# Performance work log

Hardware: AMD Instinct MI355X
Metric: run time of the kernel (lower is better)

The kernel has to match this reference:

```python
import jax, jax.numpy as jnp
import numpy as np

DECAY = 0.99
EPS = 1e-5


def setup_inputs() -> dict:
    key = jax.random.key(0)
    k1, k2 = jax.random.split(key)
    inp = jax.random.normal(k1, (32, 64, 64, 64), dtype=jnp.float32)  # [B,H,W,dim]
    embed = jax.random.normal(k2, (64, 512), dtype=jnp.float32)       # [dim, n_embed]
    cluster_size = jnp.zeros((512,), dtype=jnp.float32)
    embed_avg = embed  # buffer initialized as embed.clone() in torch
    return {"input": inp, "embed": embed, "cluster_size": cluster_size, "embed_avg": embed_avg}


def reference(input, embed, cluster_size, embed_avg):
    dim, n_embed = embed.shape
    flatten = input.reshape(-1, dim)  # [N, dim]

    # pairwise squared distances via ||f||^2 - 2 f.E + ||E||^2 -> [N, n_embed]
    dist = ((flatten ** 2).sum(1, keepdims=True)
            - 2.0 * flatten @ embed
            + (embed ** 2).sum(0, keepdims=True))
    embed_ind_flat = jnp.argmin(dist, axis=1)  # [N] (== argmax of -dist)

    # codebook lookup (F.embedding on embed.T)
    quantize = jnp.take(embed.T, embed_ind_flat, axis=0).reshape(input.shape)

    # EMA stats: one-hot sum and one-hot @ flatten expressed as scatter-adds
    ones = jnp.ones_like(embed_ind_flat, dtype=flatten.dtype)
    embed_onehot_sum = jax.ops.segment_sum(ones, embed_ind_flat, num_segments=n_embed)      # [n_embed]
    embed_sum = jax.ops.segment_sum(flatten, embed_ind_flat, num_segments=n_embed).T       # [dim, n_embed]

    new_cluster_size = cluster_size * DECAY + (1.0 - DECAY) * embed_onehot_sum
    new_embed_avg = embed_avg * DECAY + (1.0 - DECAY) * embed_sum
    n = new_cluster_size.sum()
    cs = (new_cluster_size + EPS) / (n + n_embed * EPS) * n
    new_embed = new_embed_avg / cs[None, :]

    diff = ((jax.lax.stop_gradient(quantize) - input) ** 2).mean()
    quantize_st = input + jax.lax.stop_gradient(quantize - input)  # straight-through
    embed_ind = embed_ind_flat.reshape(input.shape[:-1])

    return (quantize_st, diff, embed_ind, new_cluster_size, new_embed_avg, new_embed)
```

## Files before the change

kernel.cpp:

```cpp
#include <hip/hip_runtime.h>

typedef __attribute__((ext_vector_type(8))) short short8_t;
typedef __attribute__((ext_vector_type(4))) float f32x4;

#define N_ROWS   131072
#define DIM      64
#define NE       512
#define DECAYF   0.99f
#define OMDECAY  0.01f
#define EPSF     1e-5f
#define GAP_THR  0.02f

#define Q_OFF    0
#define DIFF_OFF 8388608
#define IND_OFF  8388609
#define CS_OFF   8519681
#define AVG_OFF  8520193
#define EMB_OFF  8552961

#define WS_ET      0
#define WS_ENORM   32768
#define WS_EN64    33280
#define WS_CSDIV   34304
#define WS_DIFF    34816
#define WS_RCNT    34817
#define WS_IDX     34818
#define WS_RLIST   165890
#define WS_BH      296964
#define WS_BL      313348
#define WS_HIST    329732
#define WS_BINBASE 330244
#define WS_CURSOR  330756
#define WS_SORTED  331268
#define WS_ACCUM   462340

__device__ __forceinline__ ushort f32_to_bf16_rn(float f) {
    unsigned u = __float_as_uint(f);
    unsigned r = (u + 0x7FFFu + ((u >> 16) & 1u)) >> 16;
    return (ushort)r;
}
__device__ __forceinline__ float bf16_to_f32(ushort h) {
    return __uint_as_float(((unsigned)h) << 16);
}

__global__ __launch_bounds__(512) void prep1_kernel(const float* __restrict__ embed,
                                                    float* __restrict__ ws) {
    const int d = blockIdx.x;
    const int c = threadIdx.x;
    float v = embed[d * NE + c];
    ws[WS_ET + c * DIM + d] = v;

    ushort hb = f32_to_bf16_rn(v);
    float  lf = v - bf16_to_f32(hb);
    ushort lb = f32_to_bf16_rn(lf);

    const int T  = c >> 4;
    const int n  = c & 15;
    const int s  = d >> 5;
    const int k8 = (d >> 3) & 3;
    const int j  = d & 7;
    const int l  = k8 * 16 + n;
    const int idx = (T * 2 + s) * 512 + l * 8 + j;
    ((ushort*)(ws + WS_BH))[idx] = hb;
    ((ushort*)(ws + WS_BL))[idx] = lb;

    if (d == 0 && c == 0) {
        ws[WS_DIFF] = 0.0f;
        ((int*)ws)[WS_RCNT] = 0;
    }
    if (d == 1) ((int*)ws)[WS_HIST + c] = 0;
    ws[WS_ACCUM + blockIdx.x * 512 + threadIdx.x] = 0.0f;
}

__global__ __launch_bounds__(256) void prep2_kernel(float* __restrict__ ws) {
    const int jcode = blockIdx.x * 4 + (threadIdx.x >> 6);
    const int d     = threadIdx.x & 63;
    float v = ws[WS_ET + jcode * DIM + d];
    double sq = (double)v * (double)v;
    #pragma unroll
    for (int off = 32; off > 0; off >>= 1) sq += __shfl_down(sq, off, 64);
    if (d == 0) {
        ws[WS_ENORM + jcode] = (float)sq;
        ((double*)(ws + WS_EN64))[jcode] = sq;
    }
}

__global__ __launch_bounds__(256) void dist_kernel(const float* __restrict__ input,
                                                   float* __restrict__ ws) {
    const int tid  = threadIdx.x;
    const int lane = tid & 63;
    const int wv   = tid >> 6;
    const int r0   = blockIdx.x * 128 + wv * 32;
    const int n15  = lane & 15;
    const int koff = (lane >> 4) * 8;

    short8_t Ahi[2][2], Alo[2][2];
    #pragma unroll
    for (int sub = 0; sub < 2; sub++) {
        const float* rp = input + (size_t)(r0 + sub * 16 + n15) * DIM + koff;
        #pragma unroll
        for (int s = 0; s < 2; s++) {
            float4 x0 = *(const float4*)(rp + s * 32);
            float4 x1 = *(const float4*)(rp + s * 32 + 4);
            float xf[8] = {x0.x, x0.y, x0.z, x0.w, x1.x, x1.y, x1.z, x1.w};
            short8_t h, l;
            #pragma unroll
            for (int e = 0; e < 8; e++) {
                ushort hb = f32_to_bf16_rn(xf[e]);
                float  lf = xf[e] - bf16_to_f32(hb);
                ushort lb = f32_to_bf16_rn(lf);
                h[e] = (short)hb;
                l[e] = (short)lb;
            }
            Ahi[sub][s] = h;
            Alo[sub][s] = l;
        }
    }

    const ushort* bhp = (const ushort*)(ws + WS_BH) + lane * 8;
    const ushort* blp = (const ushort*)(ws + WS_BL) + lane * 8;

    float m1[8], m2[8];
    int   j1[8];
    #pragma unroll
    for (int i = 0; i < 8; i++) { m1[i] = 3.4e38f; m2[i] = 3.4e38f; j1[i] = 0; }

    #pragma unroll 2
    for (int T = 0; T < 32; T++) {
        short8_t Bh0 = *(const short8_t*)(bhp + T * 1024);
        short8_t Bh1 = *(const short8_t*)(bhp + T * 1024 + 512);
        short8_t Bl0 = *(const short8_t*)(blp + T * 1024);
        short8_t Bl1 = *(const short8_t*)(blp + T * 1024 + 512);

        f32x4 aa = {0.f, 0.f, 0.f, 0.f};
        f32x4 ab = {0.f, 0.f, 0.f, 0.f};
        aa = __builtin_amdgcn_mfma_f32_16x16x32_bf16(Ahi[0][0], Bh0, aa, 0, 0, 0);
        ab = __builtin_amdgcn_mfma_f32_16x16x32_bf16(Ahi[1][0], Bh0, ab, 0, 0, 0);
        aa = __builtin_amdgcn_mfma_f32_16x16x32_bf16(Alo[0][0], Bh0, aa, 0, 0, 0);
        ab = __builtin_amdgcn_mfma_f32_16x16x32_bf16(Alo[1][0], Bh0, ab, 0, 0, 0);
        aa = __builtin_amdgcn_mfma_f32_16x16x32_bf16(Ahi[0][0], Bl0, aa, 0, 0, 0);
        ab = __builtin_amdgcn_mfma_f32_16x16x32_bf16(Ahi[1][0], Bl0, ab, 0, 0, 0);
        aa = __builtin_amdgcn_mfma_f32_16x16x32_bf16(Ahi[0][1], Bh1, aa, 0, 0, 0);
        ab = __builtin_amdgcn_mfma_f32_16x16x32_bf16(Ahi[1][1], Bh1, ab, 0, 0, 0);
        aa = __builtin_amdgcn_mfma_f32_16x16x32_bf16(Alo[0][1], Bh1, aa, 0, 0, 0);
        ab = __builtin_amdgcn_mfma_f32_16x16x32_bf16(Alo[1][1], Bh1, ab, 0, 0, 0);
        aa = __builtin_amdgcn_mfma_f32_16x16x32_bf16(Ahi[0][1], Bl1, aa, 0, 0, 0);
        ab = __builtin_amdgcn_mfma_f32_16x16x32_bf16(Ahi[1][1], Bl1, ab, 0, 0, 0);

        const float en = ws[WS_ENORM + T * 16 + n15];
        const int   jc = T * 16 + n15;
        #pragma unroll
        for (int q = 0; q < 4; q++) {
            float da = fmaf(-2.0f, aa[q], en);
            m2[q]    = fminf(m2[q], fmaxf(m1[q], da));
            j1[q]    = (da < m1[q]) ? jc : j1[q];
            m1[q]    = fminf(m1[q], da);
            float db = fmaf(-2.0f, ab[q], en);
            m2[q+4]  = fminf(m2[q+4], fmaxf(m1[q+4], db));
            j1[q+4]  = (db < m1[q+4]) ? jc : j1[q+4];
            m1[q+4]  = fminf(m1[q+4], db);
        }
    }

    #pragma unroll
    for (int off = 1; off < 16; off <<= 1) {
        #pragma unroll
        for (int i = 0; i < 8; i++) {
            float b1 = __shfl_xor(m1[i], off, 64);
            float b2 = __shfl_xor(m2[i], off, 64);
            int   bj = __shfl_xor(j1[i], off, 64);
            float a1 = m1[i];
            float nm2 = fminf(fminf(m2[i], b2), fmaxf(a1, b1));
            bool takeB = (b1 < a1) || (b1 == a1 && bj < j1[i]);
            m1[i] = takeB ? b1 : a1;
            j1[i] = takeB ? bj : j1[i];
            m2[i] = nm2;
        }
    }

    if (n15 == 0) {
        #pragma unroll
        for (int i = 0; i < 8; i++) {
            int sub = i >> 2, q = i & 3;
            int r = r0 + sub * 16 + (lane >> 4) * 4 + q;
            ((int*)ws)[WS_IDX + r] = j1[i];
            if (m2[i] - m1[i] < GAP_THR) {
                int pos = atomicAdd((int*)ws + WS_RCNT, 1);
                ((int*)ws)[WS_RLIST + pos] = r;
            }
        }
    }
}

__global__ __launch_bounds__(64) void refine_kernel(const float* __restrict__ input,
                                                    float* __restrict__ ws) {
    __shared__ float rowf[DIM];
    const int cnt  = ((const int*)ws)[WS_RCNT];
    const int lane = threadIdx.x;
    const double* en64 = (const double*)(ws + WS_EN64);
    for (int ii = blockIdx.x; ii < cnt; ii += 512) {
        const int r = ((const int*)ws)[WS_RLIST + ii];
        __syncthreads();
        rowf[lane] = input[(size_t)r * DIM + lane];
        __syncthreads();
        double bd = 1e300;
        int    bj = 0x7fffffff;
        for (int kk = 0; kk < 8; kk++) {
            int j = kk * 64 + lane;
            const float* ep = ws + WS_ET + j * DIM;
            double s = 0.0;
            #pragma unroll 8
            for (int d = 0; d < DIM; d++)
                s = fma((double)ep[d], (double)rowf[d], s);
            double dist = en64[j] - 2.0 * s;
            if (dist < bd || (dist == bd && j < bj)) { bd = dist; bj = j; }
        }
        #pragma unroll
        for (int off = 32; off > 0; off >>= 1) {
            double od = __shfl_down(bd, off, 64);
            int    oj = __shfl_down(bj, off, 64);
            if (od < bd || (od == bd && oj < bj)) { bd = od; bj = oj; }
        }
        if (lane == 0) ((int*)ws)[WS_IDX + r] = bj;
    }
}

__global__ __launch_bounds__(256) void quantize_kernel(const float* __restrict__ input,
                                                       float* __restrict__ ws,
                                                       float* __restrict__ out) {
    __shared__ int hist[NE];
    __shared__ float wsum[4];
    const int tid = threadIdx.x;
    for (int e = tid; e < NE; e += 256) hist[e] = 0;
    __syncthreads();

    const int lane = tid & 63;
    const int wv   = tid >> 6;
    const int rsub = lane >> 4;
    const int d4   = (lane & 15) * 4;
    const int base = blockIdx.x * 256;
    float dacc = 0.0f;

    #pragma unroll 4
    for (int it = 0; it < 16; it++) {
        int r = base + (it * 4 + wv) * 4 + rsub;
        int j = ((const int*)ws)[WS_IDX + r];
        float4 in4 = *(const float4*)(input + (size_t)r * DIM + d4);
        float4 q4  = *(const float4*)(ws + WS_ET + j * DIM + d4);
        *(float4*)(out + Q_OFF + (size_t)r * DIM + d4) = q4;
        float dx = q4.x - in4.x, dy = q4.y - in4.y, dz = q4.z - in4.z, dw = q4.w - in4.w;
        dacc = fmaf(dx, dx, fmaf(dy, dy, fmaf(dz, dz, fmaf(dw, dw, dacc))));
        if ((lane & 15) == 0) {
            atomicAdd(&hist[j], 1);
            out[IND_OFF + r] = (float)j;
        }
    }
    __syncthreads();

    for (int e = tid; e < NE; e += 256) {
        int h = hist[e];
        if (h) atomicAdd((int*)ws + WS_HIST + e, h);
    }

    #pragma unroll
    for (int off = 32; off > 0; off >>= 1) dacc += __shfl_down(dacc, off, 64);
    if (lane == 0) wsum[wv] = dacc;
    __syncthreads();
    if (tid == 0)
        atomicAdd(&ws[WS_DIFF], wsum[0] + wsum[1] + wsum[2] + wsum[3]);
}

__global__ __launch_bounds__(512) void scan_kernel(const float* __restrict__ cluster_size,
                                                   float* __restrict__ ws,
                                                   float* __restrict__ out) {
    __shared__ int wsums[8];
    const int t    = threadIdx.x;
    const int lane = t & 63;
    const int wv   = t >> 6;
    const int v    = ((const int*)ws)[WS_HIST + t];
    int x = v;
    #pragma unroll
    for (int off = 1; off < 64; off <<= 1) {
        int y = __shfl_up(x, off, 64);
        if (lane >= off) x += y;
    }
    if (lane == 63) wsums[wv] = x;
    __syncthreads();
    int add = 0;
    for (int w = 0; w < wv; w++) add += wsums[w];
    const int excl = x + add - v;
    ((int*)ws)[WS_BINBASE + t] = excl;
    ((int*)ws)[WS_CURSOR + t]  = excl;
    out[CS_OFF + t] = fmaf(cluster_size[t], DECAYF, OMDECAY * (float)v);
}

__global__ __launch_bounds__(512) void finalize1_kernel(float* __restrict__ ws,
                                                        float* __restrict__ out) {
    __shared__ float red[8];
    const int t = threadIdx.x;
    float v = out[CS_OFF + t];
    float s = v;
    #pragma unroll
    for (int off = 32; off > 0; off >>= 1) s += __shfl_down(s, off, 64);
    if ((t & 63) == 0) red[t >> 6] = s;
    __syncthreads();
    float n = red[0] + red[1] + red[2] + red[3] + red[4] + red[5] + red[6] + red[7];
    ws[WS_CSDIV + t] = (v + EPSF) / (n + (float)NE * EPSF) * n;
    if (t == 0) out[DIFF_OFF] = ws[WS_DIFF] * (1.0f / 8388608.0f);
}

__global__ __launch_bounds__(256) void place_kernel(float* __restrict__ ws) {
    __shared__ int lhist[NE];
    __shared__ int lbase[NE];
    __shared__ int lcur[NE];
    const int tid  = threadIdx.x;
    const int base = blockIdx.x * 256;

    for (int e = tid; e < NE; e += 256) { lhist[e] = 0; lcur[e] = 0; }
    __syncthreads();

    const int r = base + tid;
    const int j = ((const int*)ws)[WS_IDX + r];
    atomicAdd(&lhist[j], 1);
    __syncthreads();

    for (int e = tid; e < NE; e += 256)
        if (lhist[e]) lbase[e] = atomicAdd((int*)ws + WS_CURSOR + e, lhist[e]);
    __syncthreads();

    const int pos = lbase[j] + atomicAdd(&lcur[j], 1);
    ((int*)ws)[WS_SORTED + pos] = r;
}

__global__ __launch_bounds__(64) void sum_kernel(const float* __restrict__ input,
                                                 float* __restrict__ ws) {
    const int lane = threadIdx.x;
    const int i0   = blockIdx.x * 64;

    const int rv = ((const int*)ws)[WS_SORTED + i0 + lane];
    const int jv = ((const int*)ws)[WS_IDX + rv];

    float acc  = 0.0f;
    int   jcur = __shfl(jv, 0, 64);

    for (int k = 0; k < 64; k += 4) {
        int r0 = __shfl(rv, k,     64);
        int r1 = __shfl(rv, k + 1, 64);
        int r2 = __shfl(rv, k + 2, 64);
        int r3 = __shfl(rv, k + 3, 64);
        float v0 = input[(size_t)r0 * DIM + lane];
        float v1 = input[(size_t)r1 * DIM + lane];
        float v2 = input[(size_t)r2 * DIM + lane];
        float v3 = input[(size_t)r3 * DIM + lane];
        int j0 = __shfl(jv, k,     64);
        int j1 = __shfl(jv, k + 1, 64);
        int j2 = __shfl(jv, k + 2, 64);
        int j3 = __shfl(jv, k + 3, 64);

        if (j0 != jcur) { atomicAdd(&ws[WS_ACCUM + jcur * DIM + lane], acc); acc = 0.0f; jcur = j0; }
        acc += v0;
        if (j1 != jcur) { atomicAdd(&ws[WS_ACCUM + jcur * DIM + lane], acc); acc = 0.0f; jcur = j1; }
        acc += v1;
        if (j2 != jcur) { atomicAdd(&ws[WS_ACCUM + jcur * DIM + lane], acc); acc = 0.0f; jcur = j2; }
        acc += v2;
        if (j3 != jcur) { atomicAdd(&ws[WS_ACCUM + jcur * DIM + lane], acc); acc = 0.0f; jcur = j3; }
        acc += v3;
    }
    atomicAdd(&ws[WS_ACCUM + jcur * DIM + lane], acc);
}

__global__ __launch_bounds__(512) void emaout_kernel(const float* __restrict__ embed_avg,
                                                     const float* __restrict__ ws,
                                                     float* __restrict__ out) {
    const int e = blockIdx.x * 512 + threadIdx.x;
    const int d = e >> 9;
    const int j = e & (NE - 1);
    float s   = ws[WS_ACCUM + j * DIM + d];
    float avg = fmaf(embed_avg[e], DECAYF, OMDECAY * s);
    out[AVG_OFF + e] = avg;
    out[EMB_OFF + e] = avg / ws[WS_CSDIV + j];
}

extern "C" void kernel_launch(void* const* d_in, const int* in_sizes, int n_in,
                              void* d_out, int out_size, void* d_ws, size_t ws_size,
                              hipStream_t stream) {
    const float* input        = (const float*)d_in[0];
    const float* embed        = (const float*)d_in[1];
    const float* cluster_size = (const float*)d_in[2];
    const float* embed_avg    = (const float*)d_in[3];
    float* out = (float*)d_out;
    float* ws  = (float*)d_ws;

    prep1_kernel<<<64, 512, 0, stream>>>(embed, ws);
    prep2_kernel<<<128, 256, 0, stream>>>(ws);
    dist_kernel<<<N_ROWS / 128, 256, 0, stream>>>(input, ws);
    refine_kernel<<<512, 64, 0, stream>>>(input, ws);
    quantize_kernel<<<512, 256, 0, stream>>>(input, ws, out);
    scan_kernel<<<1, 512, 0, stream>>>(cluster_size, ws, out);
    finalize1_kernel<<<1, 512, 0, stream>>>(ws, out);
    place_kernel<<<512, 256, 0, stream>>>(ws);
    sum_kernel<<<N_ROWS / 64, 64, 0, stream>>>(input, ws);
    emaout_kernel<<<64, 512, 0, stream>>>(embed_avg, ws, out);
}
```

Before: 138.7 us.

## Fuse quantize into distance kernel, pack codebook index into distance bits, merge small kernels

The distance kernel now processes 64 rows per wave and seeds the MFMA accumulators with the code norms. It pre-scales the input by -2 and packs the code index into the low 9 mantissa bits, so argmin becomes a plain fminf. It also writes the quantized output, the indices, a shared-memory histogram and the diff sum directly, which removes the separate quantize kernel. Refine now patches only the rows whose index changed, the scan and finalize kernels are merged, hi/lo codebook buffers are packed together, and sum_kernel uses 256-thread blocks. Truncating the mantissa lowers distance precision, so the gap threshold is raised to send more near-tie rows to the exact refine path.

```diff
diff --git a/kernel.cpp b/kernel.cpp
--- a/kernel.cpp
+++ b/kernel.cpp
@@ -9,7 +9,7 @@
 #define DECAYF   0.99f
 #define OMDECAY  0.01f
 #define EPSF     1e-5f
-#define GAP_THR  0.02f
+#define GAP_THR  0.06f
 
 #define Q_OFF    0
 #define DIFF_OFF 8388608
@@ -26,8 +26,7 @@
 #define WS_RCNT    34817
 #define WS_IDX     34818
 #define WS_RLIST   165890
-#define WS_BH      296964
-#define WS_BL      313348
+#define WS_BPACK   296964
 #define WS_HIST    329732
 #define WS_BINBASE 330244
 #define WS_CURSOR  330756
@@ -54,15 +53,15 @@
     float  lf = v - bf16_to_f32(hb);
     ushort lb = f32_to_bf16_rn(lf);
 
-    const int T  = c >> 4;
-    const int n  = c & 15;
-    const int s  = d >> 5;
-    const int k8 = (d >> 3) & 3;
-    const int j  = d & 7;
-    const int l  = k8 * 16 + n;
-    const int idx = (T * 2 + s) * 512 + l * 8 + j;
-    ((ushort*)(ws + WS_BH))[idx] = hb;
-    ((ushort*)(ws + WS_BL))[idx] = lb;
+    const int T    = c >> 4;
+    const int n    = c & 15;
+    const int s    = d >> 5;
+    const int k8   = (d >> 3) & 3;
+    const int jj   = d & 7;
+    const int lane = k8 * 16 + n;
+    ushort* bp = (ushort*)(ws + WS_BPACK);
+    bp[T * 2048 + s * 512       + lane * 8 + jj] = hb;
+    bp[T * 2048 + (2 + s) * 512 + lane * 8 + jj] = lb;
 
     if (d == 0 && c == 0) {
         ws[WS_DIFF] = 0.0f;
@@ -85,18 +84,26 @@
     }
 }
 
-__global__ __launch_bounds__(256) void dist_kernel(const float* __restrict__ input,
-                                                   float* __restrict__ ws) {
+__global__ __launch_bounds__(256, 2) void dist_kernel(const float* __restrict__ input,
+                                                      float* __restrict__ ws,
+                                                      float* __restrict__ out) {
+    __shared__ int hist[NE];
+    __shared__ float wsum[4];
+
     const int tid  = threadIdx.x;
     const int lane = tid & 63;
     const int wv   = tid >> 6;
-    const int r0   = blockIdx.x * 128 + wv * 32;
+    const int r0   = blockIdx.x * 256 + wv * 64;
     const int n15  = lane & 15;
-    const int koff = (lane >> 4) * 8;
-
-    short8_t Ahi[2][2], Alo[2][2];
-    #pragma unroll
-    for (int sub = 0; sub < 2; sub++) {
+    const int k16  = lane >> 4;
+    const int koff = k16 * 8;
+
+    for (int e = tid; e < NE; e += 256) hist[e] = 0;
+    __syncthreads();
+
+    short8_t Ahi[4][2], Alo[4][2];
+    #pragma unroll
+    for (int sub = 0; sub < 4; sub++) {
         const float* rp = input + (size_t)(r0 + sub * 16 + n15) * DIM + koff;
         #pragma unroll
         for (int s = 0; s < 2; s++) {
@@ -106,94 +113,122 @@
             short8_t h, l;
             #pragma unroll
             for (int e = 0; e < 8; e++) {
-                ushort hb = f32_to_bf16_rn(xf[e]);
-                float  lf = xf[e] - bf16_to_f32(hb);
-                ushort lb = f32_to_bf16_rn(lf);
+                float f2 = -2.0f * xf[e];
+                ushort hb = f32_to_bf16_rn(f2);
+                float  lf = f2 - bf16_to_f32(hb);
                 h[e] = (short)hb;
-                l[e] = (short)lb;
+                l[e] = (short)f32_to_bf16_rn(lf);
             }
             Ahi[sub][s] = h;
             Alo[sub][s] = l;
         }
     }
 
-    const ushort* bhp = (const ushort*)(ws + WS_BH) + lane * 8;
-    const ushort* blp = (const ushort*)(ws + WS_BL) + lane * 8;
-
-    float m1[8], m2[8];
-    int   j1[8];
-    #pragma unroll
-    for (int i = 0; i < 8; i++) { m1[i] = 3.4e38f; m2[i] = 3.4e38f; j1[i] = 0; }
+    const ushort* bp = (const ushort*)(ws + WS_BPACK) + lane * 8;
+
+    float m1[16], m2[16];
+    #pragma unroll
+    for (int i = 0; i < 16; i++) { m1[i] = 3.4e38f; m2[i] = 3.4e38f; }
 
     #pragma unroll 2
     for (int T = 0; T < 32; T++) {
-        short8_t Bh0 = *(const short8_t*)(bhp + T * 1024);
-        short8_t Bh1 = *(const short8_t*)(bhp + T * 1024 + 512);
-        short8_t Bl0 = *(const short8_t*)(blp + T * 1024);
-        short8_t Bl1 = *(const short8_t*)(blp + T * 1024 + 512);
-
-        f32x4 aa = {0.f, 0.f, 0.f, 0.f};
-        f32x4 ab = {0.f, 0.f, 0.f, 0.f};
-        aa = __builtin_amdgcn_mfma_f32_16x16x32_bf16(Ahi[0][0], Bh0, aa, 0, 0, 0);
-        ab = __builtin_amdgcn_mfma_f32_16x16x32_bf16(Ahi[1][0], Bh0, ab, 0, 0, 0);
-        aa = __builtin_amdgcn_mfma_f32_16x16x32_bf16(Alo[0][0], Bh0, aa, 0, 0, 0);
-        ab = __builtin_amdgcn_mfma_f32_16x16x32_bf16(Alo[1][0], Bh0, ab, 0, 0, 0);
-        aa = __builtin_amdgcn_mfma_f32_16x16x32_bf16(Ahi[0][0], Bl0, aa, 0, 0, 0);
-        ab = __builtin_amdgcn_mfma_f32_16x16x32_bf16(Ahi[1][0], Bl0, ab, 0, 0, 0);
-        aa = __builtin_amdgcn_mfma_f32_16x16x32_bf16(Ahi[0][1], Bh1, aa, 0, 0, 0);
-        ab = __builtin_amdgcn_mfma_f32_16x16x32_bf16(Ahi[1][1], Bh1, ab, 0, 0, 0);
-        aa = __builtin_amdgcn_mfma_f32_16x16x32_bf16(Alo[0][1], Bh1, aa, 0, 0, 0);
-        ab = __builtin_amdgcn_mfma_f32_16x16x32_bf16(Alo[1][1], Bh1, ab, 0, 0, 0);
-        aa = __builtin_amdgcn_mfma_f32_16x16x32_bf16(Ahi[0][1], Bl1, aa, 0, 0, 0);
-        ab = __builtin_amdgcn_mfma_f32_16x16x32_bf16(Ahi[1][1], Bl1, ab, 0, 0, 0);
-
-        const float en = ws[WS_ENORM + T * 16 + n15];
-        const int   jc = T * 16 + n15;
-        #pragma unroll
-        for (int q = 0; q < 4; q++) {
-            float da = fmaf(-2.0f, aa[q], en);
-            m2[q]    = fminf(m2[q], fmaxf(m1[q], da));
-            j1[q]    = (da < m1[q]) ? jc : j1[q];
-            m1[q]    = fminf(m1[q], da);
-            float db = fmaf(-2.0f, ab[q], en);
-            m2[q+4]  = fminf(m2[q+4], fmaxf(m1[q+4], db));
-            j1[q+4]  = (db < m1[q+4]) ? jc : j1[q+4];
-            m1[q+4]  = fminf(m1[q+4], db);
+        short8_t Bh0 = *(const short8_t*)(bp + T * 2048);
+        short8_t Bh1 = *(const short8_t*)(bp + T * 2048 + 512);
+        short8_t Bl0 = *(const short8_t*)(bp + T * 2048 + 1024);
+        short8_t Bl1 = *(const short8_t*)(bp + T * 2048 + 1536);
+        const float    en = ws[WS_ENORM + T * 16 + n15];
+        const unsigned jc = (unsigned)(T * 16 + n15);
+
+        f32x4 ac[4];
+        #pragma unroll
+        for (int sub = 0; sub < 4; sub++) { f32x4 t = {en, en, en, en}; ac[sub] = t; }
+        #pragma unroll
+        for (int sub = 0; sub < 4; sub++)
+            ac[sub] = __builtin_amdgcn_mfma_f32_16x16x32_bf16(Ahi[sub][0], Bh0, ac[sub], 0, 0, 0);
+        #pragma unroll
+        for (int sub = 0; sub < 4; sub++)
+            ac[sub] = __builtin_amdgcn_mfma_f32_16x16x32_bf16(Alo[sub][0], Bh0, ac[sub], 0, 0, 0);
+        #pragma unroll
+        for (int sub = 0; sub < 4; sub++)
+            ac[sub] = __builtin_amdgcn_mfma_f32_16x16x32_bf16(Ahi[sub][1], Bh1, ac[sub], 0, 0, 0);
+        #pragma unroll
+        for (int sub = 0; sub < 4; sub++)
+            ac[sub] = __builtin_amdgcn_mfma_f32_16x16x32_bf16(Alo[sub][1], Bh1, ac[sub], 0, 0, 0);
+        #pragma unroll
+        for (int sub = 0; sub < 4; sub++)
+            ac[sub] = __builtin_amdgcn_mfma_f32_16x16x32_bf16(Ahi[sub][0], Bl0, ac[sub], 0, 0, 0);
+        #pragma unroll
+        for (int sub = 0; sub < 4; sub++)
+            ac[sub] = __builtin_amdgcn_mfma_f32_16x16x32_bf16(Ahi[sub][1], Bl1, ac[sub], 0, 0, 0);
+
+        #pragma unroll
+        for (int sub = 0; sub < 4; sub++) {
+            #pragma unroll
+            for (int q = 0; q < 4; q++) {
+                const int i = sub * 4 + q;
+                float pv = __uint_as_float((__float_as_uint(ac[sub][q]) & 0xFFFFFE00u) | jc);
+                m2[i] = fminf(m2[i], fmaxf(m1[i], pv));
+                m1[i] = fminf(m1[i], pv);
+            }
         }
     }
 
     #pragma unroll
     for (int off = 1; off < 16; off <<= 1) {
         #pragma unroll
-        for (int i = 0; i < 8; i++) {
-            float b1 = __shfl_xor(m1[i], off, 64);
-            float b2 = __shfl_xor(m2[i], off, 64);
-            int   bj = __shfl_xor(j1[i], off, 64);
-            float a1 = m1[i];
-            float nm2 = fminf(fminf(m2[i], b2), fmaxf(a1, b1));
-            bool takeB = (b1 < a1) || (b1 == a1 && bj < j1[i]);
-            m1[i] = takeB ? b1 : a1;
-            j1[i] = takeB ? bj : j1[i];
-            m2[i] = nm2;
-        }
-    }
-
-    if (n15 == 0) {
-        #pragma unroll
-        for (int i = 0; i < 8; i++) {
-            int sub = i >> 2, q = i & 3;
-            int r = r0 + sub * 16 + (lane >> 4) * 4 + q;
-            ((int*)ws)[WS_IDX + r] = j1[i];
-            if (m2[i] - m1[i] < GAP_THR) {
+        for (int i = 0; i < 16; i++) {
+            float o1 = __shfl_xor(m1[i], off, 64);
+            float o2 = __shfl_xor(m2[i], off, 64);
+            float mx = fmaxf(m1[i], o1);
+            m1[i] = fminf(m1[i], o1);
+            m2[i] = fminf(fminf(m2[i], o2), mx);
+        }
+    }
+
+    float dacc = 0.0f;
+    #pragma unroll
+    for (int i = 0; i < 16; i++) {
+        const int sub = i >> 2, q = i & 3;
+        const int r = r0 + sub * 16 + k16 * 4 + q;
+        const unsigned mb = __float_as_uint(m1[i]);
+        const int j = (int)(mb & 511u);
+
+        float4 q4 = *(const float4*)(ws + WS_ET + j * DIM + n15 * 4);
+        float4 f4 = *(const float4*)(input + (size_t)r * DIM + n15 * 4);
+        *(float4*)(out + Q_OFF + (size_t)r * DIM + n15 * 4) = q4;
+        float dx = q4.x - f4.x, dy = q4.y - f4.y, dz = q4.z - f4.z, dw = q4.w - f4.w;
+        dacc = fmaf(dx, dx, fmaf(dy, dy, fmaf(dz, dz, fmaf(dw, dw, dacc))));
+
+        if (n15 == 0) {
+            out[IND_OFF + r] = (float)j;
+            atomicAdd(&hist[j], 1);
+            float g1 = __uint_as_float(mb & 0xFFFFFE00u);
+            float g2 = __uint_as_float(__float_as_uint(m2[i]) & 0xFFFFFE00u);
+            if (g2 - g1 < GAP_THR) {
                 int pos = atomicAdd((int*)ws + WS_RCNT, 1);
                 ((int*)ws)[WS_RLIST + pos] = r;
             }
-        }
-    }
+            ((int*)ws)[WS_IDX + r] = j;
+        }
+    }
+
+    __syncthreads();
+    for (int e = tid; e < NE; e += 256) {
+        int h = hist[e];
+        if (h) atomicAdd((int*)ws + WS_HIST + e, h);
+    }
+
+    #pragma unroll
+    for (int off = 32; off > 0; off >>= 1) dacc += __shfl_down(dacc, off, 64);
+    if (lane == 0) wsum[wv] = dacc;
+    __syncthreads();
+    if (tid == 0)
+        atomicAdd(&ws[WS_DIFF], wsum[0] + wsum[1] + wsum[2] + wsum[3]);
 }
 
 __global__ __launch_bounds__(64) void refine_kernel(const float* __restrict__ input,
-                                                    float* __restrict__ ws) {
+                                                    float* __restrict__ ws,
+                                                    float* __restrict__ out) {
     __shared__ float rowf[DIM];
     const int cnt  = ((const int*)ws)[WS_RCNT];
     const int lane = threadIdx.x;
@@ -221,63 +256,32 @@
             int    oj = __shfl_down(bj, off, 64);
             if (od < bd || (od == bd && oj < bj)) { bd = od; bj = oj; }
         }
-        if (lane == 0) ((int*)ws)[WS_IDX + r] = bj;
-    }
-}
-
-__global__ __launch_bounds__(256) void quantize_kernel(const float* __restrict__ input,
-                                                       float* __restrict__ ws,
-                                                       float* __restrict__ out) {
-    __shared__ int hist[NE];
-    __shared__ float wsum[4];
-    const int tid = threadIdx.x;
-    for (int e = tid; e < NE; e += 256) hist[e] = 0;
-    __syncthreads();
-
-    const int lane = tid & 63;
-    const int wv   = tid >> 6;
-    const int rsub = lane >> 4;
-    const int d4   = (lane & 15) * 4;
-    const int base = blockIdx.x * 256;
-    float dacc = 0.0f;
-
-    #pragma unroll 4
-    for (int it = 0; it < 16; it++) {
-        int r = base + (it * 4 + wv) * 4 + rsub;
-        int j = ((const int*)ws)[WS_IDX + r];
-        float4 in4 = *(const float4*)(input + (size_t)r * DIM + d4);
-        float4 q4  = *(const float4*)(ws + WS_ET + j * DIM + d4);
-        *(float4*)(out + Q_OFF + (size_t)r * DIM + d4) = q4;
-        float dx = q4.x - in4.x, dy = q4.y - in4.y, dz = q4.z - in4.z, dw = q4.w - in4.w;
-        dacc = fmaf(dx, dx, fmaf(dy, dy, fmaf(dz, dz, fmaf(dw, dw, dacc))));
-        if ((lane & 15) == 0) {
-            atomicAdd(&hist[j], 1);
-            out[IND_OFF + r] = (float)j;
-        }
-    }
-    __syncthreads();
-
-    for (int e = tid; e < NE; e += 256) {
-        int h = hist[e];
-        if (h) atomicAdd((int*)ws + WS_HIST + e, h);
-    }
-
-    #pragma unroll
-    for (int off = 32; off > 0; off >>= 1) dacc += __shfl_down(dacc, off, 64);
-    if (lane == 0) wsum[wv] = dacc;
-    __syncthreads();
-    if (tid == 0)
-        atomicAdd(&ws[WS_DIFF], wsum[0] + wsum[1] + wsum[2] + wsum[3]);
-}
-
-__global__ __launch_bounds__(512) void scan_kernel(const float* __restrict__ cluster_size,
-                                                   float* __restrict__ ws,
-                                                   float* __restrict__ out) {
+        const int jn = __shfl(bj, 0, 64);
+        const int jold = ((const int*)ws)[WS_IDX + r];
+        if (jn != jold) {
+            out[Q_OFF + (size_t)r * DIM + lane] = ws[WS_ET + jn * DIM + lane];
+            if (lane == 0) {
+                ((int*)ws)[WS_IDX + r] = jn;
+                out[IND_OFF + r] = (float)jn;
+                atomicAdd((int*)ws + WS_HIST + jold, -1);
+                atomicAdd((int*)ws + WS_HIST + jn, 1);
+            }
+        }
+    }
+}
+
+__global__ __launch_bounds__(512) void scanfin_kernel(const float* __restrict__ cluster_size,
+                                                      float* __restrict__ ws,
+                                                      float* __restrict__ out) {
     __shared__ int wsums[8];
+    __shared__ float red[8];
     const int t    = threadIdx.x;
     const int lane = t & 63;
     const int wv   = t >> 6;
     const int v    = ((const int*)ws)[WS_HIST + t];
+    const float csnew = fmaf(cluster_size[t], DECAYF, OMDECAY * (float)v);
+    out[CS_OFF + t] = csnew;
+
     int x = v;
     #pragma unroll
     for (int off = 1; off < 64; off <<= 1) {
@@ -285,27 +289,21 @@
         if (lane >= off) x += y;
     }
     if (lane == 63) wsums[wv] = x;
-    __syncthreads();
+
+    float s = csnew;
+    #pragma unroll
+    for (int off = 32; off > 0; off >>= 1) s += __shfl_down(s, off, 64);
+    if (lane == 0) red[wv] = s;
+    __syncthreads();
+
     int add = 0;
     for (int w = 0; w < wv; w++) add += wsums[w];
     const int excl = x + add - v;
     ((int*)ws)[WS_BINBASE + t] = excl;
     ((int*)ws)[WS_CURSOR + t]  = excl;
-    out[CS_OFF + t] = fmaf(cluster_size[t], DECAYF, OMDECAY * (float)v);
-}
-
-__global__ __launch_bounds__(512) void finalize1_kernel(float* __restrict__ ws,
-                                                        float* __restrict__ out) {
-    __shared__ float red[8];
-    const int t = threadIdx.x;
-    float v = out[CS_OFF + t];
-    float s = v;
-    #pragma unroll
-    for (int off = 32; off > 0; off >>= 1) s += __shfl_down(s, off, 64);
-    if ((t & 63) == 0) red[t >> 6] = s;
-    __syncthreads();
+
     float n = red[0] + red[1] + red[2] + red[3] + red[4] + red[5] + red[6] + red[7];
-    ws[WS_CSDIV + t] = (v + EPSF) / (n + (float)NE * EPSF) * n;
+    ws[WS_CSDIV + t] = (csnew + EPSF) / (n + (float)NE * EPSF) * n;
     if (t == 0) out[DIFF_OFF] = ws[WS_DIFF] * (1.0f / 8388608.0f);
 }
 
@@ -332,10 +330,11 @@
     ((int*)ws)[WS_SORTED + pos] = r;
 }
 
-__global__ __launch_bounds__(64) void sum_kernel(const float* __restrict__ input,
-                                                 float* __restrict__ ws) {
-    const int lane = threadIdx.x;
-    const int i0   = blockIdx.x * 64;
+__global__ __launch_bounds__(256) void sum_kernel(const float* __restrict__ input,
+                                                  float* __restrict__ ws) {
+    const int lane = threadIdx.x & 63;
+    const int wv   = threadIdx.x >> 6;
+    const int i0   = (blockIdx.x * 4 + wv) * 64;
 
     const int rv = ((const int*)ws)[WS_SORTED + i0 + lane];
     const int jv = ((const int*)ws)[WS_IDX + rv];
@@ -393,12 +392,10 @@
 
     prep1_kernel<<<64, 512, 0, stream>>>(embed, ws);
     prep2_kernel<<<128, 256, 0, stream>>>(ws);
-    dist_kernel<<<N_ROWS / 128, 256, 0, stream>>>(input, ws);
-    refine_kernel<<<512, 64, 0, stream>>>(input, ws);
-    quantize_kernel<<<512, 256, 0, stream>>>(input, ws, out);
-    scan_kernel<<<1, 512, 0, stream>>>(cluster_size, ws, out);
-    finalize1_kernel<<<1, 512, 0, stream>>>(ws, out);
-    place_kernel<<<512, 256, 0, stream>>>(ws);
-    sum_kernel<<<N_ROWS / 64, 64, 0, stream>>>(input, ws);
+    dist_kernel<<<N_ROWS / 256, 256, 0, stream>>>(input, ws, out);
+    refine_kernel<<<512, 64, 0, stream>>>(input, ws, out);
+    scanfin_kernel<<<1, 512, 0, stream>>>(cluster_size, ws, out);
+    place_kernel<<<N_ROWS / 256, 256, 0, stream>>>(ws);
+    sum_kernel<<<N_ROWS / 256, 256, 0, stream>>>(input, ws);
     emaout_kernel<<<64, 512, 0, stream>>>(embed_avg, ws, out);
 }
```

New measurement: 161.0 us. +16.1%, slower.
